# Kernel optimization log

Hardware: AMD Instinct MI355X
Metric: run time of the kernel (lower is better)

The kernel has to match this reference:

```python
import jax, jax.numpy as jnp
import numpy as np


def _lstm_cell(x, h, c, W_ih, W_hh, b_ih, b_hh):
    # torch.nn.LSTMCell: gates ordered (i, f, g, o)
    gates = x @ W_ih.T + h @ W_hh.T + b_ih + b_hh
    i, f, g, o = jnp.split(gates, 4, axis=-1)
    c_next = jax.nn.sigmoid(f) * c + jax.nn.sigmoid(i) * jnp.tanh(g)
    h_next = jax.nn.sigmoid(o) * jnp.tanh(c_next)
    return h_next, c_next


def setup_inputs() -> dict:
    key = jax.random.key(0)
    ks = jax.random.split(key, 6)
    B, T, N, K_SUP, E = 64, 128, 128, 8, 512
    scale = 1.0 / np.sqrt(E)
    return {
        "targets": jax.random.normal(ks[0], (B, T, E), jnp.float32),
        "support_embeddings": jax.random.normal(ks[1], (B, N, K_SUP, E), jnp.float32),
        "W_ih": jax.random.normal(ks[2], (4 * E, E), jnp.float32) * scale,
        "W_hh": jax.random.normal(ks[3], (4 * E, E), jnp.float32) * scale,
        "b_ih": jnp.zeros((4 * E,), jnp.float32),
        "b_hh": jnp.zeros((4 * E,), jnp.float32),
        "processing_steps": 10,
    }


def reference(targets, support_embeddings, W_ih, W_hh, b_ih, b_hh, processing_steps):
    B, T, E = targets.shape
    _, N, K_SUP, _ = support_embeddings.shape
    x = targets.reshape(B * T, E)  # flattened targets fed every step

    def step(carry, _):
        h_prev, c_prev = carry
        h_next, c_next = _lstm_cell(x, h_prev, c_prev, W_ih, W_hh, b_ih, b_hh)
        h_next = h_next + x  # residual add of the input encoding
        # attention scores between previous hidden state and support set
        hq = h_prev.reshape(B, T, E)
        scores = jnp.einsum('bte,bnke->btnk', hq, support_embeddings)
        attn = jax.nn.softmax(scores.reshape(B, T, N * K_SUP), axis=-1)
        attn = attn.reshape(B, T, N, K_SUP)
        # attention read over the support embeddings
        r = jnp.einsum('btnk,bnke->bte', attn, support_embeddings)
        h_next = h_next + r.reshape(B * T, E)
        return (h_next, c_next), None

    h0 = jnp.zeros_like(x)
    c0 = jnp.zeros_like(x)
    (h_fin, _), _ = jax.lax.scan(step, (h0, c0), None, length=processing_steps)
    return h_fin.reshape(B, T, E)
```

## Files before the change

### kernel.cpp

```cpp
#include <hip/hip_runtime.h>

#define DI __device__ __forceinline__
typedef unsigned short u16;
typedef __bf16 v8bf  __attribute__((ext_vector_type(8)));
typedef float  f32x4 __attribute__((ext_vector_type(4)));

DI u16 f2bf(float f){ unsigned u=__float_as_uint(f); return (u16)((u + 0x7fffu + ((u>>16)&1u))>>16); }
DI float bf2f(u16 u){ return __uint_as_float(((unsigned)u)<<16); }
DI float sigf(float x){ return 1.f/(1.f+__expf(-x)); }

DI void gload16(const void* g, void* l){
  __builtin_amdgcn_global_load_lds((const __attribute__((address_space(1))) unsigned int*)g,
                                   (__attribute__((address_space(3))) unsigned int*)l, 16, 0, 0);
}

template<int N> DI void waitv(){ asm volatile("s_waitcnt vmcnt(%0)" :: "n"(N) : "memory"); }

DI void xswz(int& bx, int& by){
  int gx=gridDim.x, nwg=gx*gridDim.y;
  int bid=blockIdx.y*gx+blockIdx.x;
  int cpx=nwg>>3;
  int sw=(bid&7)*cpx+(bid>>3);
  bx=sw%gx; by=sw/gx;
}

template<int NCH>
DI void stage(const u16* __restrict__ G, int ld, u16* Ls, int tid){
  #pragma unroll
  for(int j=0;j<NCH;++j){
    int ci=j*512+tid; int r=ci>>3, ch=ci&7;
    gload16(G + (size_t)r*ld + ((ch^(r&7))<<3), Ls + ci*8);
  }
}
DI void stage_gate(const u16* __restrict__ W, int e0, int k0, u16* Ls, int tid){
  #pragma unroll
  for(int j=0;j<4;++j){
    int ci=j*512+tid; int r=ci>>3, ch=ci&7;
    int row=((r>>4)&3)*512 + e0 + (r>>6)*16 + (r&15);
    gload16(W + (size_t)row*512 + k0 + ((ch^(r&7))<<3), Ls + ci*8);
  }
}

template<int NF>
DI void mma_tile(const u16* As, const u16* Bs, f32x4 (&acc)[4][NF], int wr,int wc,int l15,int kh){
  #pragma unroll
  for(int ks=0;ks<2;++ks){
    int co=(((ks*4+kh)^(l15&7))<<3);
    v8bf a[4], b[NF];
    #pragma unroll
    for(int mi=0;mi<4;++mi) a[mi]=*(const v8bf*)(As + (wr*64+mi*16+l15)*64 + co);
    #pragma unroll
    for(int n=0;n<NF;++n)   b[n] =*(const v8bf*)(Bs + (wc*(NF*16)+n*16+l15)*64 + co);
    __builtin_amdgcn_s_setprio(1);
    #pragma unroll
    for(int mi=0;mi<4;++mi){
      #pragma unroll
      for(int n=0;n<NF;++n)
        acc[mi][n]=__builtin_amdgcn_mfma_f32_16x16x32_bf16(a[mi],b[n],acc[mi][n],0,0,0);
    }
    __builtin_amdgcn_s_setprio(0);
  }
}

#define PIPELINE(NT, LODS) \
  STG(0); STG(1); \
  waitv<LODS>(); __builtin_amdgcn_s_barrier(); __builtin_amdgcn_sched_barrier(0); \
  _Pragma("clang loop unroll(disable)") \
  for(int t=0;t<NT;++t){ \
    if(t+2<NT) STG(t+2); \
    CMP(t%3); \
    if(t+1<NT){ \
      if(t+2<NT) waitv<LODS>(); else waitv<0>(); \
      __builtin_amdgcn_s_barrier(); __builtin_amdgcn_sched_barrier(0); \
    } \
  }

#define ACC_INIT(NF) f32x4 acc[4][NF]; \
  _Pragma("unroll") for(int i_=0;i_<4;i_++){ _Pragma("unroll") for(int n_=0;n_<NF;n_++) acc[i_][n_]=(f32x4){0.f,0.f,0.f,0.f}; }

#define WAVE_IDS int tid=threadIdx.x, w=tid>>6, wr=w>>2, wc=w&3, lane=tid&63, l15=lane&15, kh=lane>>4; (void)lane;

__global__ void k_split(const float* __restrict__ in, u16* __restrict__ hi, u16* __restrict__ lo, int n4){
  int i=blockIdx.x*256+threadIdx.x;
  if(i<n4){
    float4 v=((const float4*)in)[i];
    ushort4 h,l;
    h.x=f2bf(v.x); l.x=f2bf(v.x-bf2f(h.x));
    h.y=f2bf(v.y); l.y=f2bf(v.y-bf2f(h.y));
    h.z=f2bf(v.z); l.z=f2bf(v.z-bf2f(h.z));
    h.w=f2bf(v.w); l.w=f2bf(v.w-bf2f(h.w));
    ((ushort4*)hi)[i]=h; ((ushort4*)lo)[i]=l;
  }
}

__global__ __launch_bounds__(256) void k_transpose(const float* __restrict__ U,
    u16* __restrict__ uth, u16* __restrict__ utl){
  __shared__ float T[64][65];
  int b=blockIdx.z, j0=blockIdx.y*64, e0=blockIdx.x*64;
  int tid=threadIdx.x;
  const float* Ub = U + ((size_t)b*1024 + j0)*512 + e0;
  #pragma unroll
  for(int it=0;it<16;++it){
    int idx=it*256+tid; int j=idx>>6, e=idx&63;
    T[j][e]=Ub[(size_t)j*512+e];
  }
  __syncthreads();
  size_t ob=((size_t)b*512 + e0)*1024 + j0;
  #pragma unroll
  for(int it=0;it<16;++it){
    int idx=it*256+tid; int e=idx>>6, j=idx&63;
    float v=T[j][e];
    u16 hb=f2bf(v);
    uth[ob+(size_t)e*1024+j]=hb;
    utl[ob+(size_t)e*1024+j]=f2bf(v-bf2f(hb));
  }
}

__global__ __launch_bounds__(512,2) void k_gx(const u16* __restrict__ xh, const u16* __restrict__ xl,
    const u16* __restrict__ wh, const u16* __restrict__ wl,
    const float* __restrict__ bih, const float* __restrict__ bhh,
    u16* __restrict__ gxh, u16* __restrict__ gxl)
{
  __shared__ __attribute__((aligned(16))) u16 As[3][128*64];
  __shared__ __attribute__((aligned(16))) u16 Bs[3][256*64];
  int bx,by; xswz(bx,by);
  int n0=bx*256, m0=by*128;
  WAVE_IDS
  ACC_INIT(4)
  auto STG=[&](int tt){
    int ps=tt>>3, k0=(tt&7)<<6, sl=tt%3;
    const u16* Aq=(ps==1)?xl:xh;
    const u16* Bq=(ps==2)?wl:wh;
    stage<2>(Aq+(size_t)m0*512+k0,512,As[sl],tid);
    stage<4>(Bq+(size_t)n0*512+k0,512,Bs[sl],tid);
  };
  auto CMP=[&](int sl){ mma_tile<4>(As[sl],Bs[sl],acc,wr,wc,l15,kh); };
  PIPELINE(24,6)
  #pragma unroll
  for(int mi=0;mi<4;++mi){
    #pragma unroll
    for(int i=0;i<4;++i){
      int row=m0+wr*64+mi*16+kh*4+i;
      #pragma unroll
      for(int n=0;n<4;++n){
        int col=n0+wc*64+n*16+l15;
        float v=acc[mi][n][i]+bih[col]+bhh[col];
        u16 hb=f2bf(v);
        gxh[(size_t)row*2048+col]=hb;
        gxl[(size_t)row*2048+col]=f2bf(v-bf2f(hb));
      }
    }
  }
}

__global__ __launch_bounds__(512,2) void k_gates(const u16* __restrict__ hh, const u16* __restrict__ hl,
    const u16* __restrict__ whh_h, const u16* __restrict__ whh_l,
    const u16* __restrict__ gxh, const u16* __restrict__ gxl,
    const float* __restrict__ x, float* __restrict__ c, float* __restrict__ htmp)
{
  __shared__ __attribute__((aligned(16))) u16 As[3][128*64];
  __shared__ __attribute__((aligned(16))) u16 Bs[3][256*64];
  int bx,by; xswz(bx,by);
  int e0=bx*64, m0=by*128;
  WAVE_IDS
  ACC_INIT(4)
  auto STG=[&](int tt){
    int ps=tt>>3, k0=(tt&7)<<6, sl=tt%3;
    const u16* Aq=(ps==1)?hl:hh;
    const u16* Bq=(ps==2)?whh_l:whh_h;
    stage<2>(Aq+(size_t)m0*512+k0,512,As[sl],tid);
    stage_gate(Bq,e0,k0,Bs[sl],tid);
  };
  auto CMP=[&](int sl){ mma_tile<4>(As[sl],Bs[sl],acc,wr,wc,l15,kh); };
  PIPELINE(24,6)
  #pragma unroll
  for(int mi=0;mi<4;++mi){
    #pragma unroll
    for(int i=0;i<4;++i){
      int row=m0+wr*64+mi*16+kh*4+i;
      size_t gb=(size_t)row*2048;
      int e=e0+wc*16+l15;
      float gi=acc[mi][0][i]+bf2f(gxh[gb+e])     +bf2f(gxl[gb+e]);
      float gf=acc[mi][1][i]+bf2f(gxh[gb+512+e]) +bf2f(gxl[gb+512+e]);
      float gg=acc[mi][2][i]+bf2f(gxh[gb+1024+e])+bf2f(gxl[gb+1024+e]);
      float go=acc[mi][3][i]+bf2f(gxh[gb+1536+e])+bf2f(gxl[gb+1536+e]);
      size_t off=(size_t)row*512+e;
      float cn=sigf(gf)*c[off]+sigf(gi)*tanhf(gg);
      c[off]=cn;
      htmp[off]=sigf(go)*tanhf(cn)+x[off];
    }
  }
}

__global__ __launch_bounds__(512,2) void k_scores(const u16* __restrict__ hh, const u16* __restrict__ hl,
    const u16* __restrict__ uh, const u16* __restrict__ ul, float* __restrict__ S)
{
  __shared__ __attribute__((aligned(16))) u16 As[3][128*64];
  __shared__ __attribute__((aligned(16))) u16 Bs[3][256*64];
  int bx,by; xswz(bx,by);
  int b=by, n0=bx*256, m0=b*128;
  WAVE_IDS
  ACC_INIT(4)
  size_t ub=(size_t)b*1024*512+(size_t)n0*512;
  auto STG=[&](int tt){
    int ps=tt>>3, k0=(tt&7)<<6, sl=tt%3;
    const u16* Aq=(ps==1)?hl:hh;
    const u16* Bq=(ps==2)?ul:uh;
    stage<2>(Aq+(size_t)m0*512+k0,512,As[sl],tid);
    stage<4>(Bq+ub+k0,512,Bs[sl],tid);
  };
  auto CMP=[&](int sl){ mma_tile<4>(As[sl],Bs[sl],acc,wr,wc,l15,kh); };
  PIPELINE(24,6)
  #pragma unroll
  for(int mi=0;mi<4;++mi){
    #pragma unroll
    for(int i=0;i<4;++i){
      int row=m0+wr*64+mi*16+kh*4+i;
      #pragma unroll
      for(int n=0;n<4;++n)
        S[(size_t)row*1024 + n0+wc*64+n*16+l15]=acc[mi][n][i];
    }
  }
}

__global__ __launch_bounds__(256) void k_softmax(float* S){
  int row=blockIdx.x*4+(threadIdx.x>>6);
  int lane=threadIdx.x&63;
  float* sr=S+(size_t)row*1024;
  float4 v[4]; float m=-3.0e38f;
  #pragma unroll
  for(int i=0;i<4;++i){
    v[i]=((const float4*)sr)[i*64+lane];
    m=fmaxf(m,fmaxf(fmaxf(v[i].x,v[i].y),fmaxf(v[i].z,v[i].w)));
  }
  #pragma unroll
  for(int s=32;s;s>>=1) m=fmaxf(m,__shfl_xor(m,s));
  float sum=0.f; float pv[16];
  #pragma unroll
  for(int i=0;i<4;++i){
    pv[i*4+0]=__expf(v[i].x-m); pv[i*4+1]=__expf(v[i].y-m);
    pv[i*4+2]=__expf(v[i].z-m); pv[i*4+3]=__expf(v[i].w-m);
    sum+=pv[i*4+0]+pv[i*4+1]+pv[i*4+2]+pv[i*4+3];
  }
  #pragma unroll
  for(int s=32;s;s>>=1) sum+=__shfl_xor(sum,s);
  float inv=1.f/sum;
  u16* ar=(u16*)S + (size_t)row*2048;
  #pragma unroll
  for(int i=0;i<4;++i){
    ushort4 h,l;
    float p;
    p=pv[i*4+0]*inv; h.x=f2bf(p); l.x=f2bf(p-bf2f(h.x));
    p=pv[i*4+1]*inv; h.y=f2bf(p); l.y=f2bf(p-bf2f(h.y));
    p=pv[i*4+2]*inv; h.z=f2bf(p); l.z=f2bf(p-bf2f(h.z));
    p=pv[i*4+3]*inv; h.w=f2bf(p); l.w=f2bf(p-bf2f(h.w));
    *(ushort4*)(ar + i*256+lane*4)        = h;
    *(ushort4*)(ar + 1024 + i*256+lane*4) = l;
  }
}

__global__ __launch_bounds__(512,2) void k_rcomb(const u16* __restrict__ attn, const u16* __restrict__ uth,
    const u16* __restrict__ utl, const float* __restrict__ htmp, float* hout,
    u16* __restrict__ hh, u16* __restrict__ hl)
{
  __shared__ __attribute__((aligned(16))) u16 As[3][128*64];
  __shared__ __attribute__((aligned(16))) u16 Bs[3][128*64];
  int bx,by; xswz(bx,by);
  int b=by, n0=bx*128, m0=b*128;
  WAVE_IDS
  ACC_INIT(2)
  size_t ub=(size_t)b*512*1024+(size_t)n0*1024;
  auto STG=[&](int tt){
    int ps=tt>>4, k0=(tt&15)<<6, sl=tt%3;
    const u16* Aq=attn+(size_t)m0*2048+((ps==1)?1024:0);
    const u16* Bq=(ps==2)?utl:uth;
    stage<2>(Aq+k0,2048,As[sl],tid);
    stage<2>(Bq+ub+k0,1024,Bs[sl],tid);
  };
  auto CMP=[&](int sl){ mma_tile<2>(As[sl],Bs[sl],acc,wr,wc,l15,kh); };
  PIPELINE(48,4)
  #pragma unroll
  for(int mi=0;mi<4;++mi){
    #pragma unroll
    for(int i=0;i<4;++i){
      int row=m0+wr*64+mi*16+kh*4+i;
      #pragma unroll
      for(int n=0;n<2;++n){
        int e=n0+wc*32+n*16+l15;
        size_t off=(size_t)row*512+e;
        float v=htmp[off]+acc[mi][n][i];
        if(hout) hout[off]=v;
        u16 hb=f2bf(v);
        hh[off]=hb; hl[off]=f2bf(v-bf2f(hb));
      }
    }
  }
}

extern "C" void kernel_launch(void* const* d_in, const int* in_sizes, int n_in,
                              void* d_out, int out_size, void* d_ws, size_t ws_size,
                              hipStream_t stream)
{
  const float* x   = (const float*)d_in[0];
  const float* U   = (const float*)d_in[1];
  const float* wihf= (const float*)d_in[2];
  const float* whhf= (const float*)d_in[3];
  const float* bih = (const float*)d_in[4];
  const float* bhh = (const float*)d_in[5];

  const size_t MB=1048576;
  char* p=(char*)d_ws;
  u16*   u_hi =(u16*)(p+  0*MB);
  u16*   u_lo =(u16*)(p+ 64*MB);
  u16*   ut_hi=(u16*)(p+128*MB);
  u16*   ut_lo=(u16*)(p+192*MB);
  u16*   gx_hi=(u16*)(p+256*MB);
  u16*   gx_lo=(u16*)(p+288*MB);
  float* S    =(float*)(p+320*MB);
  u16*   xhi  =(u16*)(p+320*MB);
  u16*   xlo  =(u16*)(p+336*MB);
  float* c    =(float*)(p+352*MB);
  float* htmp =(float*)(p+368*MB);
  u16*   wihh =(u16*)(p+368*MB);
  u16*   wihl =(u16*)(p+370*MB);
  u16*   h_hi =(u16*)(p+384*MB);
  u16*   h_lo =(u16*)(p+392*MB);
  u16*   whhh =(u16*)(p+400*MB);
  u16*   whhl =(u16*)(p+402*MB);
  if (ws_size < 404*MB){
    hipMemsetAsync(d_out, 0x3F, (size_t)out_size*4, stream);
    return;
  }

  k_split<<<4096 ,256,0,stream>>>(x,    xhi,  xlo,  1048576);
  k_split<<<1024 ,256,0,stream>>>(wihf, wihh, wihl, 262144);
  k_split<<<1024 ,256,0,stream>>>(whhf, whhh, whhl, 262144);
  k_split<<<32768,256,0,stream>>>(U,    u_hi, u_lo, 8388608);
  k_transpose<<<dim3(8,16,64),256,0,stream>>>(U, ut_hi, ut_lo);
  k_gx<<<dim3(8,64),512,0,stream>>>(xhi, xlo, wihh, wihl, bih, bhh, gx_hi, gx_lo);
  hipMemsetAsync(c,    0, 16*MB, stream);
  hipMemsetAsync(h_hi, 0,  8*MB, stream);
  hipMemsetAsync(h_lo, 0,  8*MB, stream);

  for (int s=0;s<10;++s){
    k_gates  <<<dim3(8,64),512,0,stream>>>(h_hi,h_lo, whhh,whhl, gx_hi,gx_lo, x, c, htmp);
    k_scores <<<dim3(4,64),512,0,stream>>>(h_hi,h_lo, u_hi,u_lo, S);
    k_softmax<<<2048      ,256,0,stream>>>(S);
    k_rcomb  <<<dim3(4,64),512,0,stream>>>((const u16*)S, ut_hi,ut_lo, htmp,
                                           (s==9)?(float*)d_out:nullptr, h_hi,h_lo);
  }
}
```

Before: 2.715 ms.

## Fuse hi/lo split-bf16 passes into one K loop with single-buffered 128x128 tiles

```diff
diff --git a/kernel.cpp b/kernel.cpp
--- a/kernel.cpp
+++ b/kernel.cpp
@@ -13,8 +13,6 @@
   __builtin_amdgcn_global_load_lds((const __attribute__((address_space(1))) unsigned int*)g,
                                    (__attribute__((address_space(3))) unsigned int*)l, 16, 0, 0);
 }
-
-template<int N> DI void waitv(){ asm volatile("s_waitcnt vmcnt(%0)" :: "n"(N) : "memory"); }
 
 DI void xswz(int& bx, int& by){
   int gx=gridDim.x, nwg=gx*gridDim.y;
@@ -24,61 +22,74 @@
   bx=sw%gx; by=sw/gx;
 }
 
-template<int NCH>
-DI void stage(const u16* __restrict__ G, int ld, u16* Ls, int tid){
-  #pragma unroll
-  for(int j=0;j<NCH;++j){
-    int ci=j*512+tid; int r=ci>>3, ch=ci&7;
+DI void stage128(const u16* __restrict__ G, int ld, u16* Ls, int tid){
+  #pragma unroll
+  for(int j=0;j<4;++j){
+    int ci=j*256+tid; int r=ci>>3, ch=ci&7;
     gload16(G + (size_t)r*ld + ((ch^(r&7))<<3), Ls + ci*8);
   }
 }
 DI void stage_gate(const u16* __restrict__ W, int e0, int k0, u16* Ls, int tid){
   #pragma unroll
   for(int j=0;j<4;++j){
-    int ci=j*512+tid; int r=ci>>3, ch=ci&7;
+    int ci=j*256+tid; int r=ci>>3, ch=ci&7;
     int row=((r>>4)&3)*512 + e0 + (r>>6)*16 + (r&15);
     gload16(W + (size_t)row*512 + k0 + ((ch^(r&7))<<3), Ls + ci*8);
   }
 }
 
-template<int NF>
-DI void mma_tile(const u16* As, const u16* Bs, f32x4 (&acc)[4][NF], int wr,int wc,int l15,int kh){
-  #pragma unroll
-  for(int ks=0;ks<2;++ks){
-    int co=(((ks*4+kh)^(l15&7))<<3);
-    v8bf a[4], b[NF];
-    #pragma unroll
-    for(int mi=0;mi<4;++mi) a[mi]=*(const v8bf*)(As + (wr*64+mi*16+l15)*64 + co);
-    #pragma unroll
-    for(int n=0;n<NF;++n)   b[n] =*(const v8bf*)(Bs + (wc*(NF*16)+n*16+l15)*64 + co);
+DI void kcompute(const u16* AhS,const u16* AlS,const u16* BhS,const u16* BlS,
+                 f32x4 (&acc)[4][4], int wr,int wc,int l15,int kh){
+  int r7=l15&7;
+  int co0=((kh^r7)<<3), co1=(((4+kh)^r7)<<3);
+  v8bf ah[4][2], al[4][2];
+  #pragma unroll
+  for(int mi=0;mi<4;++mi){
+    int ro=(wr*64+mi*16+l15)*64;
+    ah[mi][0]=*(const v8bf*)(AhS+ro+co0); ah[mi][1]=*(const v8bf*)(AhS+ro+co1);
+    al[mi][0]=*(const v8bf*)(AlS+ro+co0); al[mi][1]=*(const v8bf*)(AlS+ro+co1);
+  }
+  #pragma unroll
+  for(int n=0;n<4;++n){
+    int ro=(wc*64+n*16+l15)*64;
+    v8bf bh0=*(const v8bf*)(BhS+ro+co0), bh1=*(const v8bf*)(BhS+ro+co1);
+    v8bf bl0=*(const v8bf*)(BlS+ro+co0), bl1=*(const v8bf*)(BlS+ro+co1);
     __builtin_amdgcn_s_setprio(1);
     #pragma unroll
-    for(int mi=0;mi<4;++mi){
-      #pragma unroll
-      for(int n=0;n<NF;++n)
-        acc[mi][n]=__builtin_amdgcn_mfma_f32_16x16x32_bf16(a[mi],b[n],acc[mi][n],0,0,0);
-    }
+    for(int mi=0;mi<4;++mi) acc[mi][n]=__builtin_amdgcn_mfma_f32_16x16x32_bf16(ah[mi][0],bh0,acc[mi][n],0,0,0);
+    #pragma unroll
+    for(int mi=0;mi<4;++mi) acc[mi][n]=__builtin_amdgcn_mfma_f32_16x16x32_bf16(ah[mi][1],bh1,acc[mi][n],0,0,0);
+    #pragma unroll
+    for(int mi=0;mi<4;++mi) acc[mi][n]=__builtin_amdgcn_mfma_f32_16x16x32_bf16(al[mi][0],bh0,acc[mi][n],0,0,0);
+    #pragma unroll
+    for(int mi=0;mi<4;++mi) acc[mi][n]=__builtin_amdgcn_mfma_f32_16x16x32_bf16(al[mi][1],bh1,acc[mi][n],0,0,0);
+    #pragma unroll
+    for(int mi=0;mi<4;++mi) acc[mi][n]=__builtin_amdgcn_mfma_f32_16x16x32_bf16(ah[mi][0],bl0,acc[mi][n],0,0,0);
+    #pragma unroll
+    for(int mi=0;mi<4;++mi) acc[mi][n]=__builtin_amdgcn_mfma_f32_16x16x32_bf16(ah[mi][1],bl1,acc[mi][n],0,0,0);
     __builtin_amdgcn_s_setprio(0);
   }
 }
 
-#define PIPELINE(NT, LODS) \
-  STG(0); STG(1); \
-  waitv<LODS>(); __builtin_amdgcn_s_barrier(); __builtin_amdgcn_sched_barrier(0); \
+#define LDS_DECL \
+  __shared__ __attribute__((aligned(16))) u16 AhS[128*64]; \
+  __shared__ __attribute__((aligned(16))) u16 AlS[128*64]; \
+  __shared__ __attribute__((aligned(16))) u16 BhS[128*64]; \
+  __shared__ __attribute__((aligned(16))) u16 BlS[128*64];
+
+#define ACC_INIT f32x4 acc[4][4]; \
+  _Pragma("unroll") for(int i_=0;i_<4;i_++){ _Pragma("unroll") for(int n_=0;n_<4;n_++) acc[i_][n_]=(f32x4){0.f,0.f,0.f,0.f}; }
+
+#define WAVE_IDS int tid=threadIdx.x, w=tid>>6, wr=w>>1, wc=w&1, lane=tid&63, l15=lane&15, kh=lane>>4; (void)lane;
+
+#define KLOOP(NT, STG) \
   _Pragma("clang loop unroll(disable)") \
   for(int t=0;t<NT;++t){ \
-    if(t+2<NT) STG(t+2); \
-    CMP(t%3); \
-    if(t+1<NT){ \
-      if(t+2<NT) waitv<LODS>(); else waitv<0>(); \
-      __builtin_amdgcn_s_barrier(); __builtin_amdgcn_sched_barrier(0); \
-    } \
-  }
-
-#define ACC_INIT(NF) f32x4 acc[4][NF]; \
-  _Pragma("unroll") for(int i_=0;i_<4;i_++){ _Pragma("unroll") for(int n_=0;n_<NF;n_++) acc[i_][n_]=(f32x4){0.f,0.f,0.f,0.f}; }
-
-#define WAVE_IDS int tid=threadIdx.x, w=tid>>6, wr=w>>2, wc=w&3, lane=tid&63, l15=lane&15, kh=lane>>4; (void)lane;
+    STG(t); \
+    __syncthreads(); \
+    kcompute(AhS,AlS,BhS,BlS,acc,wr,wc,l15,kh); \
+    __syncthreads(); \
+  }
 
 __global__ void k_split(const float* __restrict__ in, u16* __restrict__ hi, u16* __restrict__ lo, int n4){
   int i=blockIdx.x*256+threadIdx.x;
@@ -116,26 +127,22 @@
   }
 }
 
-__global__ __launch_bounds__(512,2) void k_gx(const u16* __restrict__ xh, const u16* __restrict__ xl,
+__global__ __launch_bounds__(256,2) void k_gx(const u16* __restrict__ xh, const u16* __restrict__ xl,
     const u16* __restrict__ wh, const u16* __restrict__ wl,
     const float* __restrict__ bih, const float* __restrict__ bhh,
     u16* __restrict__ gxh, u16* __restrict__ gxl)
 {
-  __shared__ __attribute__((aligned(16))) u16 As[3][128*64];
-  __shared__ __attribute__((aligned(16))) u16 Bs[3][256*64];
+  LDS_DECL
   int bx,by; xswz(bx,by);
-  int n0=bx*256, m0=by*128;
+  int n0=bx*128, m0=by*128;
   WAVE_IDS
-  ACC_INIT(4)
-  auto STG=[&](int tt){
-    int ps=tt>>3, k0=(tt&7)<<6, sl=tt%3;
-    const u16* Aq=(ps==1)?xl:xh;
-    const u16* Bq=(ps==2)?wl:wh;
-    stage<2>(Aq+(size_t)m0*512+k0,512,As[sl],tid);
-    stage<4>(Bq+(size_t)n0*512+k0,512,Bs[sl],tid);
-  };
-  auto CMP=[&](int sl){ mma_tile<4>(As[sl],Bs[sl],acc,wr,wc,l15,kh); };
-  PIPELINE(24,6)
+  ACC_INIT
+  const u16* Ah=xh+(size_t)m0*512; const u16* Al=xl+(size_t)m0*512;
+  const u16* Bh=wh+(size_t)n0*512; const u16* Bl=wl+(size_t)n0*512;
+  #define STG_GX(t) { int k0=(t)<<6; \
+    stage128(Ah+k0,512,AhS,tid); stage128(Al+k0,512,AlS,tid); \
+    stage128(Bh+k0,512,BhS,tid); stage128(Bl+k0,512,BlS,tid); }
+  KLOOP(8, STG_GX)
   #pragma unroll
   for(int mi=0;mi<4;++mi){
     #pragma unroll
@@ -153,26 +160,21 @@
   }
 }
 
-__global__ __launch_bounds__(512,2) void k_gates(const u16* __restrict__ hh, const u16* __restrict__ hl,
+__global__ __launch_bounds__(256,2) void k_gates(const u16* __restrict__ hh, const u16* __restrict__ hl,
     const u16* __restrict__ whh_h, const u16* __restrict__ whh_l,
     const u16* __restrict__ gxh, const u16* __restrict__ gxl,
     const float* __restrict__ x, float* __restrict__ c, float* __restrict__ htmp)
 {
-  __shared__ __attribute__((aligned(16))) u16 As[3][128*64];
-  __shared__ __attribute__((aligned(16))) u16 Bs[3][256*64];
+  LDS_DECL
   int bx,by; xswz(bx,by);
-  int e0=bx*64, m0=by*128;
+  int e0=bx*32, m0=by*128;
   WAVE_IDS
-  ACC_INIT(4)
-  auto STG=[&](int tt){
-    int ps=tt>>3, k0=(tt&7)<<6, sl=tt%3;
-    const u16* Aq=(ps==1)?hl:hh;
-    const u16* Bq=(ps==2)?whh_l:whh_h;
-    stage<2>(Aq+(size_t)m0*512+k0,512,As[sl],tid);
-    stage_gate(Bq,e0,k0,Bs[sl],tid);
-  };
-  auto CMP=[&](int sl){ mma_tile<4>(As[sl],Bs[sl],acc,wr,wc,l15,kh); };
-  PIPELINE(24,6)
+  ACC_INIT
+  const u16* Ah=hh+(size_t)m0*512; const u16* Al=hl+(size_t)m0*512;
+  #define STG_GATES(t) { int k0=(t)<<6; \
+    stage128(Ah+k0,512,AhS,tid); stage128(Al+k0,512,AlS,tid); \
+    stage_gate(whh_h,e0,k0,BhS,tid); stage_gate(whh_l,e0,k0,BlS,tid); }
+  KLOOP(8, STG_GATES)
   #pragma unroll
   for(int mi=0;mi<4;++mi){
     #pragma unroll
@@ -192,25 +194,21 @@
   }
 }
 
-__global__ __launch_bounds__(512,2) void k_scores(const u16* __restrict__ hh, const u16* __restrict__ hl,
+__global__ __launch_bounds__(256,2) void k_scores(const u16* __restrict__ hh, const u16* __restrict__ hl,
     const u16* __restrict__ uh, const u16* __restrict__ ul, float* __restrict__ S)
 {
-  __shared__ __attribute__((aligned(16))) u16 As[3][128*64];
-  __shared__ __attribute__((aligned(16))) u16 Bs[3][256*64];
+  LDS_DECL
   int bx,by; xswz(bx,by);
-  int b=by, n0=bx*256, m0=b*128;
+  int b=by, n0=bx*128, m0=b*128;
   WAVE_IDS
-  ACC_INIT(4)
+  ACC_INIT
   size_t ub=(size_t)b*1024*512+(size_t)n0*512;
-  auto STG=[&](int tt){
-    int ps=tt>>3, k0=(tt&7)<<6, sl=tt%3;
-    const u16* Aq=(ps==1)?hl:hh;
-    const u16* Bq=(ps==2)?ul:uh;
-    stage<2>(Aq+(size_t)m0*512+k0,512,As[sl],tid);
-    stage<4>(Bq+ub+k0,512,Bs[sl],tid);
-  };
-  auto CMP=[&](int sl){ mma_tile<4>(As[sl],Bs[sl],acc,wr,wc,l15,kh); };
-  PIPELINE(24,6)
+  const u16* Ah=hh+(size_t)m0*512; const u16* Al=hl+(size_t)m0*512;
+  const u16* Bh=uh+ub; const u16* Bl=ul+ub;
+  #define STG_SC(t) { int k0=(t)<<6; \
+    stage128(Ah+k0,512,AhS,tid); stage128(Al+k0,512,AlS,tid); \
+    stage128(Bh+k0,512,BhS,tid); stage128(Bl+k0,512,BlS,tid); }
+  KLOOP(8, STG_SC)
   #pragma unroll
   for(int mi=0;mi<4;++mi){
     #pragma unroll
@@ -259,34 +257,31 @@
   }
 }
 
-__global__ __launch_bounds__(512,2) void k_rcomb(const u16* __restrict__ attn, const u16* __restrict__ uth,
+__global__ __launch_bounds__(256,2) void k_rcomb(const u16* __restrict__ attn, const u16* __restrict__ uth,
     const u16* __restrict__ utl, const float* __restrict__ htmp, float* hout,
     u16* __restrict__ hh, u16* __restrict__ hl)
 {
-  __shared__ __attribute__((aligned(16))) u16 As[3][128*64];
-  __shared__ __attribute__((aligned(16))) u16 Bs[3][128*64];
+  LDS_DECL
   int bx,by; xswz(bx,by);
   int b=by, n0=bx*128, m0=b*128;
   WAVE_IDS
-  ACC_INIT(2)
+  ACC_INIT
   size_t ub=(size_t)b*512*1024+(size_t)n0*1024;
-  auto STG=[&](int tt){
-    int ps=tt>>4, k0=(tt&15)<<6, sl=tt%3;
-    const u16* Aq=attn+(size_t)m0*2048+((ps==1)?1024:0);
-    const u16* Bq=(ps==2)?utl:uth;
-    stage<2>(Aq+k0,2048,As[sl],tid);
-    stage<2>(Bq+ub+k0,1024,Bs[sl],tid);
-  };
-  auto CMP=[&](int sl){ mma_tile<2>(As[sl],Bs[sl],acc,wr,wc,l15,kh); };
-  PIPELINE(48,4)
+  const u16* Ah=attn+(size_t)m0*2048;
+  const u16* Al=Ah+1024;
+  const u16* Bh=uth+ub; const u16* Bl=utl+ub;
+  #define STG_RC(t) { int k0=(t)<<6; \
+    stage128(Ah+k0,2048,AhS,tid); stage128(Al+k0,2048,AlS,tid); \
+    stage128(Bh+k0,1024,BhS,tid); stage128(Bl+k0,1024,BlS,tid); }
+  KLOOP(16, STG_RC)
   #pragma unroll
   for(int mi=0;mi<4;++mi){
     #pragma unroll
     for(int i=0;i<4;++i){
       int row=m0+wr*64+mi*16+kh*4+i;
       #pragma unroll
-      for(int n=0;n<2;++n){
-        int e=n0+wc*32+n*16+l15;
+      for(int n=0;n<4;++n){
+        int e=n0+wc*64+n*16+l15;
         size_t off=(size_t)row*512+e;
         float v=htmp[off]+acc[mi][n][i];
         if(hout) hout[off]=v;
@@ -337,16 +332,16 @@
   k_split<<<1024 ,256,0,stream>>>(whhf, whhh, whhl, 262144);
   k_split<<<32768,256,0,stream>>>(U,    u_hi, u_lo, 8388608);
   k_transpose<<<dim3(8,16,64),256,0,stream>>>(U, ut_hi, ut_lo);
-  k_gx<<<dim3(8,64),512,0,stream>>>(xhi, xlo, wihh, wihl, bih, bhh, gx_hi, gx_lo);
+  k_gx<<<dim3(16,64),256,0,stream>>>(xhi, xlo, wihh, wihl, bih, bhh, gx_hi, gx_lo);
   hipMemsetAsync(c,    0, 16*MB, stream);
   hipMemsetAsync(h_hi, 0,  8*MB, stream);
   hipMemsetAsync(h_lo, 0,  8*MB, stream);
 
   for (int s=0;s<10;++s){
-    k_gates  <<<dim3(8,64),512,0,stream>>>(h_hi,h_lo, whhh,whhl, gx_hi,gx_lo, x, c, htmp);
-    k_scores <<<dim3(4,64),512,0,stream>>>(h_hi,h_lo, u_hi,u_lo, S);
-    k_softmax<<<2048      ,256,0,stream>>>(S);
-    k_rcomb  <<<dim3(4,64),512,0,stream>>>((const u16*)S, ut_hi,ut_lo, htmp,
-                                           (s==9)?(float*)d_out:nullptr, h_hi,h_lo);
-  }
-}
+    k_gates  <<<dim3(16,64),256,0,stream>>>(h_hi,h_lo, whhh,whhl, gx_hi,gx_lo, x, c, htmp);
+    k_scores <<<dim3(8,64) ,256,0,stream>>>(h_hi,h_lo, u_hi,u_lo, S);
+    k_softmax<<<2048       ,256,0,stream>>>(S);
+    k_rcomb  <<<dim3(4,64) ,256,0,stream>>>((const u16*)S, ut_hi,ut_lo, htmp,
+                                            (s==9)?(float*)d_out:nullptr, h_hi,h_lo);
+  }
+}
```

Measured after the change: 2.238 ms. -17.6%, faster.
